# Kernel optimization log

Measured on AMD Instinct MI355X. Metric: run time of the kernel, lower is better.

## Reference

```python
import jax, jax.numpy as jnp
import numpy as np

B, T, F, H = 128, 256, 64, 512

def glorot(key, shape):
    fan_in, fan_out = shape[0], shape[1]
    lim = jnp.sqrt(6.0 / (fan_in + fan_out))
    return jax.random.uniform(key, shape, jnp.float32, -lim, lim)

def setup_inputs() -> dict:
    key = jax.random.key(0)
    ks = jax.random.split(key, 8)
    x = jax.random.normal(ks[0], (B, T, F), jnp.float32)
    W1 = glorot(ks[1], (F, H)); b1 = jnp.zeros((H,), jnp.float32)
    Wx1 = glorot(ks[2], (H, 4 * H)); Wh1 = glorot(ks[3], (H, 4 * H))
    blstm1 = jnp.concatenate([jnp.zeros((H,)), jnp.ones((H,)), jnp.zeros((2 * H,))]).astype(jnp.float32)  # keras unit_forget_bias
    Wx2 = glorot(ks[4], (H, 4 * H)); Wh2 = glorot(ks[5], (H, 4 * H))
    blstm2 = jnp.concatenate([jnp.zeros((H,)), jnp.ones((H,)), jnp.zeros((2 * H,))]).astype(jnp.float32)
    gamma = jnp.ones((H,), jnp.float32); beta = jnp.zeros((H,), jnp.float32)
    W2 = glorot(ks[6], (H, H // 2)); b2 = jnp.zeros((H // 2,), jnp.float32)
    W3 = glorot(ks[7], (H // 2, 1)); b3 = jnp.zeros((1,), jnp.float32)
    return dict(x=x, W1=W1, b1=b1, Wx1=Wx1, Wh1=Wh1, blstm1=blstm1,
                Wx2=Wx2, Wh2=Wh2, blstm2=blstm2, gamma=gamma, beta=beta,
                W2=W2, b2=b2, W3=W3, b3=b3)

def lstm(x, Wx, Wh, b):
    # x: [B, T, Din] -> sequence of hidden states [B, T, H] and last h [B, H]
    h_dim = Wh.shape[0]
    xg = jnp.einsum('btd,dg->btg', x, Wx) + b  # precompute input contributions [B,T,4H]
    def step(carry, xt):
        h, c = carry
        g = xt + h @ Wh
        i, f, cb, o = jnp.split(g, 4, axis=-1)
        i = jax.nn.sigmoid(i); f = jax.nn.sigmoid(f); o = jax.nn.sigmoid(o)
        c = f * c + i * jnp.tanh(cb)
        h = o * jnp.tanh(c)
        return (h, c), h
    init = (jnp.zeros((x.shape[0], h_dim), x.dtype), jnp.zeros((x.shape[0], h_dim), x.dtype))
    (h_last, _), hs = jax.lax.scan(step, init, jnp.swapaxes(xg, 0, 1))
    return jnp.swapaxes(hs, 0, 1), h_last

def reference(x, W1, b1, Wx1, Wh1, blstm1, Wx2, Wh2, blstm2, gamma, beta, W2, b2, W3, b3):
    h = x @ W1 + b1                                  # dense1 [B,T,H]
    # spectral_norm lambda: L2-normalize last axis, scale by sqrt(H)
    norm = jnp.linalg.norm(h, axis=-1, keepdims=True)
    h = h / jnp.maximum(norm, 1e-12) * jnp.sqrt(jnp.float32(h.shape[-1]))
    seq, _ = lstm(h, Wx1, Wh1, blstm1)               # lstm1 return_sequences
    _, h2 = lstm(seq, Wx2, Wh2, blstm2)              # lstm2 last output [B,H]
    mu = jnp.mean(h2, axis=-1, keepdims=True)
    var = jnp.mean((h2 - mu) ** 2, axis=-1, keepdims=True)
    h2 = (h2 - mu) * jax.lax.rsqrt(var + 1e-3) * gamma + beta  # keras LayerNorm eps=1e-3
    h3 = jax.nn.relu(h2 @ W2 + b2)
    return h3 @ W3 + b3                               # [B,1]
```

## Files before the change

kernel.cpp:

```cpp
#include <hip/hip_runtime.h>
#include <hip/hip_bf16.h>
#include <math.h>

#define B_ 128
#define T_ 256
#define F_ 64
#define H_ 512
#define G4_ 2048

#define XB0_OFF 0
#define XB1_OFF 32768
#define HB_OFF  65536
#define GLD_OFF 98304
#define SMEM_TOTAL 115712

typedef __attribute__((ext_vector_type(8))) short bf16x8;
typedef __attribute__((ext_vector_type(4))) float f32x4;

__device__ __forceinline__ void coh_store_u32(unsigned* p, unsigned v) {
  __hip_atomic_store(p, v, __ATOMIC_RELAXED, __HIP_MEMORY_SCOPE_AGENT);
}
__device__ __forceinline__ unsigned coh_load_u32(const unsigned* p) {
  return __hip_atomic_load(p, __ATOMIC_RELAXED, __HIP_MEMORY_SCOPE_AGENT);
}
__device__ __forceinline__ void rawbar() { __builtin_amdgcn_s_barrier(); }

__device__ __forceinline__ void async_ld16(const void* g, void* l) {
  __builtin_amdgcn_global_load_lds(
      (const __attribute__((address_space(1))) void*)g,
      (__attribute__((address_space(3))) void*)l, 16, 0, 0);
}
__device__ __forceinline__ void async_ld16c(const void* g, void* l) {
  __builtin_amdgcn_global_load_lds(
      (const __attribute__((address_space(1))) void*)g,
      (__attribute__((address_space(3))) void*)l, 16, 0, 17);
}

__device__ __forceinline__ float fsig(float x) {
  float e = __builtin_amdgcn_exp2f(-1.44269504089f * x);
  return __builtin_amdgcn_rcpf(1.f + e);
}
__device__ __forceinline__ float ftanh(float x) {
  float ax = __builtin_fabsf(x);
  float e = __builtin_amdgcn_exp2f(-2.88539008177f * ax);
  float r = (1.f - e) * __builtin_amdgcn_rcpf(1.f + e);
  return __builtin_copysignf(r, x);
}

__global__ __launch_bounds__(256) void transpose_cast_k(
    const float* __restrict__ s0, const float* __restrict__ s1,
    const float* __restrict__ s2, const float* __restrict__ s3,
    __hip_bfloat16* __restrict__ dst)
{
  __shared__ float lds[64][65];
  const float* src = (blockIdx.z == 0) ? s0 : (blockIdx.z == 1) ? s1 : (blockIdx.z == 2) ? s2 : s3;
  __hip_bfloat16* d = dst + (size_t)blockIdx.z * (G4_ * H_);
  int n0 = blockIdx.x * 64, k0 = blockIdx.y * 64;
  int tx = threadIdx.x & 63, ty = threadIdx.x >> 6;
#pragma unroll
  for (int r = 0; r < 16; r++) { int k = r * 4 + ty; lds[k][tx] = src[(size_t)(k0 + k) * G4_ + n0 + tx]; }
  __syncthreads();
#pragma unroll
  for (int r = 0; r < 16; r++) { int n = r * 4 + ty; d[(size_t)(n0 + n) * H_ + k0 + tx] = __float2bfloat16(lds[tx][n]); }
}

__global__ void prep_misc_k(const float* __restrict__ w1, __hip_bfloat16* __restrict__ w1b,
                            float* __restrict__ zbase, int nzero)
{
  int i = blockIdx.x * blockDim.x + threadIdx.x;
  int stride = gridDim.x * blockDim.x;
  for (int k = i; k < F_ * H_; k += stride) w1b[k] = __float2bfloat16(w1[k]);
  for (int k = i; k < nzero; k += stride) zbase[k] = 0.f;
}

__global__ __launch_bounds__(512) void dense1_k(
    const float* __restrict__ x, const __hip_bfloat16* __restrict__ w1b,
    const float* __restrict__ b1, __hip_bfloat16* __restrict__ h0)
{
  __shared__ float red[8];
  int j = threadIdx.x;
  int wave = j >> 6, lane = j & 63;
  float wcol[64];
#pragma unroll
  for (int k = 0; k < 64; k++) wcol[k] = __bfloat162float(w1b[k * H_ + j]);
  float bj = b1[j];
  for (int r = 0; r < 32; r++) {
    int row = blockIdx.x * 32 + r;
    const float* xr = x + (size_t)row * F_;
    float acc = bj;
#pragma unroll
    for (int k = 0; k < 64; k++) acc += xr[k] * wcol[k];
    float ss = acc * acc;
#pragma unroll
    for (int o = 32; o; o >>= 1) ss += __shfl_down(ss, o);
    if (lane == 0) red[wave] = ss;
    __syncthreads();
    float tot = red[0] + red[1] + red[2] + red[3] + red[4] + red[5] + red[6] + red[7];
    float sc = sqrtf(512.f) / fmaxf(sqrtf(tot), 1e-12f);
    h0[(size_t)row * H_ + j] = __float2bfloat16(acc * sc);
    __syncthreads();
  }
}

#define RUN_CHAIN(BASEPTR, W0, W1, A0, A1)                                    \
  {                                                                           \
    const char* _cb = (const char*)(BASEPTR);                                 \
    _Pragma("unroll")                                                         \
    for (int kc = 0; kc < 8; kc++) {                                          \
      bf16x8 _av = *(const bf16x8*)(_cb + ((mh * 16 + kh * 8 + kc) << 10) + (lane << 4)); \
      A0 = __builtin_amdgcn_mfma_f32_16x16x32_bf16(_av, W0[kc], A0, 0, 0, 0); \
      A1 = __builtin_amdgcn_mfma_f32_16x16x32_bf16(_av, W1[kc], A1, 0, 0, 0); \
    }                                                                         \
  }

__global__ __launch_bounds__(512, 2) void lstm_fused_k(
    const __hip_bfloat16* __restrict__ h0,
    __hip_bfloat16* __restrict__ seq,
    const __hip_bfloat16* __restrict__ wh1, const __hip_bfloat16* __restrict__ wx1,
    const float* __restrict__ bl1,
    const __hip_bfloat16* __restrict__ wh2, const __hip_bfloat16* __restrict__ wx2,
    const float* __restrict__ bl2,
    __hip_bfloat16* __restrict__ h1A, __hip_bfloat16* __restrict__ h1B,
    __hip_bfloat16* __restrict__ h2A, __hip_bfloat16* __restrict__ h2B,
    float* __restrict__ h2f,
    unsigned* flags)
{
  extern __shared__ char smem[];
  float* gld = (float*)(smem + GLD_OFF);
  const int tid = threadIdx.x;
  const int wave = tid >> 6;
  const int lane = tid & 63;
  const int lr = lane & 15;
  const int lk = lane >> 4;
  const int bid = blockIdx.x;
  const int grp = bid >> 7;
  const int lid = bid & 127;
  const int bb = lid & 3;
  const int bu = lid >> 2;
  const int m0 = bb * 32;
  const int u0 = bu * 16;

  const int kh = wave >> 2;
  const int mh = (wave >> 1) & 1;
  const int gp = wave & 1;

  const __hip_bfloat16* Wht = grp ? wh2 : wh1;
  const __hip_bfloat16* Wxt = grp ? wx2 : wx1;
  const __hip_bfloat16* xsrc = grp ? (const __hip_bfloat16*)seq : h0;
  const float* bias = grp ? bl2 : bl1;
  __hip_bfloat16* hgA = grp ? h2A : h1A;
  __hip_bfloat16* hgB = grp ? h2B : h1B;
  unsigned* dflags = flags + bb * 64;
  unsigned* ownf = dflags + (grp << 5);
  const int myflag = (grp << 5) | bu;

  bf16x8 wh_0[8], wh_1[8], wx_0[8], wx_1[8];
  {
    const size_t c0 = (size_t)((gp * 2 + 0) * 512 + u0 + lr) * H_ + kh * 256 + lk * 8;
    const size_t c1 = (size_t)((gp * 2 + 1) * 512 + u0 + lr) * H_ + kh * 256 + lk * 8;
#pragma unroll
    for (int kc = 0; kc < 8; kc++) {
      wh_0[kc] = *(const bf16x8*)(Wht + c0 + kc * 32);
      wh_1[kc] = *(const bf16x8*)(Wht + c1 + kc * 32);
      wx_0[kc] = *(const bf16x8*)(Wxt + c0 + kc * 32);
      wx_1[kc] = *(const bf16x8*)(Wxt + c1 + kc * 32);
    }
#pragma unroll
    for (int kc = 0; kc < 8; kc++) {
      asm volatile("" : "+v"(wh_0[kc]), "+v"(wh_1[kc]), "+v"(wx_0[kc]), "+v"(wx_1[kc]));
    }
  }

  const int m_e = tid >> 3, up_e = tid & 7;
  float br0[2], br1[2], br2[2], br3[2];
  float2 creg = {0.f, 0.f};
  if (tid < 256) {
#pragma unroll
    for (int c = 0; c < 2; c++) {
      br0[c] = bias[0 * 512 + u0 + 2 * up_e + c];
      br1[c] = bias[1 * 512 + u0 + 2 * up_e + c];
      br2[c] = bias[2 * 512 + u0 + 2 * up_e + c];
      br3[c] = bias[3 * 512 + u0 + 2 * up_e + c];
    }
  }

  char* xb0 = smem + XB0_OFF;
  char* xb1 = smem + XB1_OFF;

  auto issue_x = [&](int t, char* xb) {
#pragma unroll
    for (int j = 0; j < 4; j++) {
      const int c = wave * 4 + j;
      const __hip_bfloat16* g = xsrc +
          ((size_t)(m0 + (c >> 4) * 16 + lr) * T_ + t) * H_ + (c & 15) * 32 + lk * 8;
      if (grp) async_ld16c(g, xb + c * 1024);
      else     async_ld16(g, xb + c * 1024);
    }
  };
  auto issue_h = [&](const __hip_bfloat16* hsrc) {
#pragma unroll
    for (int j = 0; j < 4; j++) {
      const int c = wave * 4 + j;
      async_ld16c(hsrc + (size_t)(m0 + (c >> 4) * 16 + lr) * H_ + (c & 15) * 32 + lk * 8,
                  smem + HB_OFF + c * 1024);
    }
  };
  auto spin = [&](const unsigned* base, unsigned tgt) {
    if (lane < 32) {
      const unsigned* p = base + lane;
      while (coh_load_u32(p) < tgt) __builtin_amdgcn_s_sleep(2);
    }
  };
  auto publish = [&](unsigned v) {
    if (tid == 0) coh_store_u32(&dflags[myflag], v);
  };
  auto write_gld = [&](f32x4 s0, f32x4 s1) {
    float* d0 = gld + ((kh * 4 + gp * 2 + 0) * 32 + mh * 16 + lk * 4) * 17 + lr;
    float* d1 = gld + ((kh * 4 + gp * 2 + 1) * 32 + mh * 16 + lk * 4) * 17 + lr;
#pragma unroll
    for (int r = 0; r < 4; r++) { d0[r * 17] = s0[r]; d1[r * 17] = s1[r]; }
  };
  auto elem = [&](int u, __hip_bfloat16* hout) {
    if (tid < 256) {
      float gv0[2], gv1[2], gv2[2], gv3[2];
#pragma unroll
      for (int c = 0; c < 2; c++) {
        const int o = m_e * 17 + 2 * up_e + c;
        gv0[c] = gld[(0 * 32) * 17 + o] + gld[(4 * 32) * 17 + o] + br0[c];
        gv1[c] = gld[(1 * 32) * 17 + o] + gld[(5 * 32) * 17 + o] + br1[c];
        gv2[c] = gld[(2 * 32) * 17 + o] + gld[(6 * 32) * 17 + o] + br2[c];
        gv3[c] = gld[(3 * 32) * 17 + o] + gld[(7 * 32) * 17 + o] + br3[c];
      }
      float i0 = fsig(gv0[0]), i1 = fsig(gv0[1]);
      float f0 = fsig(gv1[0]), f1 = fsig(gv1[1]);
      float cb0 = ftanh(gv2[0]), cb1 = ftanh(gv2[1]);
      float o0 = fsig(gv3[0]), o1 = fsig(gv3[1]);
      float cn0 = f0 * creg.x + i0 * cb0;
      float cn1 = f1 * creg.y + i1 * cb1;
      creg.x = cn0; creg.y = cn1;
      float hv0 = o0 * ftanh(cn0), hv1 = o1 * ftanh(cn1);
      union { __hip_bfloat16 h[2]; unsigned u32; } pk;
      pk.h[0] = __float2bfloat16(hv0);
      pk.h[1] = __float2bfloat16(hv1);
      const int row = m0 + m_e, col = u0 + 2 * up_e;
      coh_store_u32((unsigned*)hout + ((size_t)row * H_ + col) / 2, pk.u32);
      if (grp == 0) {
        coh_store_u32((unsigned*)seq + (((size_t)row * T_ + u) * H_ + col) / 2, pk.u32);
      } else if (u == T_ - 1) {
        float2 hv = {hv0, hv1};
        *(float2*)(h2f + (size_t)row * H_ + col) = hv;
      }
    }
  };

  f32x4 axc0 = {0.f,0.f,0.f,0.f}, axc1 = {0.f,0.f,0.f,0.f};
  f32x4 axn0, axn1, ah0, ah1;

  if (grp) spin(dflags, 2u);
  issue_x(0, xb0);
  issue_x(1, xb1);
  asm volatile("s_waitcnt vmcnt(4)" ::: "memory");
  rawbar();
  __builtin_amdgcn_sched_barrier(0);
  RUN_CHAIN(xb0, wx_0, wx_1, axc0, axc1);
  write_gld(axc0, axc1);
  asm volatile("s_waitcnt lgkmcnt(0)" ::: "memory");
  rawbar();
  __builtin_amdgcn_sched_barrier(0);
  if (grp) spin(dflags, 3u);
  elem(0, hgA);
  issue_x(2, xb0);
  asm volatile("s_waitcnt vmcnt(4)" ::: "memory");
  rawbar();
  publish(1u);
  axc0 = (f32x4){0.f,0.f,0.f,0.f}; axc1 = (f32x4){0.f,0.f,0.f,0.f};
  RUN_CHAIN(xb1, wx_0, wx_1, axc0, axc1);

  for (int u = 1; u < T_; u++) {
    __hip_bfloat16* hsrc = ((u - 1) & 1) ? hgB : hgA;
    __hip_bfloat16* hout = (u & 1) ? hgB : hgA;
    const bool pf = (u <= T_ - 3);

    spin(ownf, (unsigned)u);
    issue_h(hsrc);
    if (grp && pf) spin(dflags, (unsigned)(u + 3));
    asm volatile("s_waitcnt vmcnt(4)" ::: "memory");
    rawbar();
    __builtin_amdgcn_sched_barrier(0);
    if (u < T_ - 1) {
      axn0 = (f32x4){0.f,0.f,0.f,0.f}; axn1 = (f32x4){0.f,0.f,0.f,0.f};
      char* xb = ((u + 1) & 1) ? xb1 : xb0;
      RUN_CHAIN(xb, wx_0, wx_1, axn0, axn1);
    }
    asm volatile("s_waitcnt vmcnt(0)" ::: "memory");
    rawbar();
    __builtin_amdgcn_sched_barrier(0);
    ah0 = (f32x4){0.f,0.f,0.f,0.f}; ah1 = (f32x4){0.f,0.f,0.f,0.f};
    RUN_CHAIN(smem + HB_OFF, wh_0, wh_1, ah0, ah1);
    write_gld(axc0 + ah0, axc1 + ah1);
    asm volatile("s_waitcnt lgkmcnt(0)" ::: "memory");
    rawbar();
    __builtin_amdgcn_sched_barrier(0);
    elem(u, hout);
    if (pf) {
      issue_x(u + 2, (u & 1) ? xb1 : xb0);
      asm volatile("s_waitcnt vmcnt(4)" ::: "memory");
    } else {
      asm volatile("s_waitcnt vmcnt(0)" ::: "memory");
    }
    rawbar();
    publish((unsigned)(u + 1));
    axc0 = axn0; axc1 = axn1;
  }
}

__global__ __launch_bounds__(256) void final_k(
    const float* __restrict__ h2, const float* __restrict__ gamma, const float* __restrict__ beta,
    const float* __restrict__ W2, const float* __restrict__ b2,
    const float* __restrict__ W3, const float* __restrict__ b3, float* __restrict__ out)
{
  __shared__ float y[512];
  __shared__ float redS[4], redQ[4], redP[4];
  int b = blockIdx.x, tid = threadIdx.x;
  int wave = tid >> 6, lane = tid & 63;
  float v0 = h2[b * H_ + tid], v1 = h2[b * H_ + 256 + tid];
  float s = v0 + v1, q = v0 * v0 + v1 * v1;
#pragma unroll
  for (int o = 32; o; o >>= 1) { s += __shfl_down(s, o); q += __shfl_down(q, o); }
  if (lane == 0) { redS[wave] = s; redQ[wave] = q; }
  __syncthreads();
  float tot = redS[0] + redS[1] + redS[2] + redS[3];
  float totq = redQ[0] + redQ[1] + redQ[2] + redQ[3];
  float mu = tot * (1.f / 512.f);
  float var = totq * (1.f / 512.f) - mu * mu;
  float rs = rsqrtf(var + 1e-3f);
  y[tid]       = (v0 - mu) * rs * gamma[tid] + beta[tid];
  y[tid + 256] = (v1 - mu) * rs * gamma[tid + 256] + beta[tid + 256];
  __syncthreads();
  float acc = b2[tid];
  for (int k = 0; k < 512; k++) acc += y[k] * W2[k * 256 + tid];
  float pv = fmaxf(acc, 0.f) * W3[tid];
#pragma unroll
  for (int o = 32; o; o >>= 1) pv += __shfl_down(pv, o);
  if (lane == 0) redP[wave] = pv;
  __syncthreads();
  if (tid == 0) out[b] = redP[0] + redP[1] + redP[2] + redP[3] + b3[0];
}

extern "C" void kernel_launch(void* const* d_in, const int* in_sizes, int n_in,
                              void* d_out, int out_size, void* d_ws, size_t ws_size,
                              hipStream_t stream)
{
  (void)in_sizes; (void)n_in; (void)out_size; (void)ws_size;
  const float* x    = (const float*)d_in[0];
  const float* W1   = (const float*)d_in[1];
  const float* b1   = (const float*)d_in[2];
  const float* Wx1  = (const float*)d_in[3];
  const float* Wh1  = (const float*)d_in[4];
  const float* bl1  = (const float*)d_in[5];
  const float* Wx2  = (const float*)d_in[6];
  const float* Wh2  = (const float*)d_in[7];
  const float* bl2  = (const float*)d_in[8];
  const float* gam  = (const float*)d_in[9];
  const float* bet  = (const float*)d_in[10];
  const float* W2   = (const float*)d_in[11];
  const float* b2   = (const float*)d_in[12];
  const float* W3   = (const float*)d_in[13];
  const float* b3   = (const float*)d_in[14];

  char* p = (char*)d_ws;
  const size_t MB = 1024 * 1024;
  __hip_bfloat16* wx1t = (__hip_bfloat16*)(p + 0 * MB);
  __hip_bfloat16* wh1t = (__hip_bfloat16*)(p + 2 * MB);
  __hip_bfloat16* wx2t = (__hip_bfloat16*)(p + 4 * MB);
  __hip_bfloat16* wh2t = (__hip_bfloat16*)(p + 6 * MB);
  __hip_bfloat16* w1b  = (__hip_bfloat16*)(p + 8 * MB);
  __hip_bfloat16* h0   = (__hip_bfloat16*)(p + 9 * MB);
  __hip_bfloat16* seq  = (__hip_bfloat16*)(p + 41 * MB);
  char* st = p + 73 * MB;
  __hip_bfloat16* h1A = (__hip_bfloat16*)st;
  __hip_bfloat16* h1B = h1A + B_ * H_;
  __hip_bfloat16* h2A = h1B + B_ * H_;
  __hip_bfloat16* h2B = h2A + B_ * H_;
  float* h2f = (float*)(st + 512 * 1024);
  unsigned* flags = (unsigned*)(st + 512 * 1024 + 256 * 1024);
  int nzero = (int)((512 * 1024 + 256 * 1024 + 4096) / 4);

  transpose_cast_k<<<dim3(32, 8, 4), 256, 0, stream>>>(Wx1, Wh1, Wx2, Wh2, wx1t);
  prep_misc_k<<<256, 256, 0, stream>>>(W1, w1b, (float*)st, nzero);
  dense1_k<<<1024, 512, 0, stream>>>(x, w1b, b1, h0);

  void* args[] = { (void*)&h0, (void*)&seq,
                   (void*)&wh1t, (void*)&wx1t, (void*)&bl1,
                   (void*)&wh2t, (void*)&wx2t, (void*)&bl2,
                   (void*)&h1A, (void*)&h1B, (void*)&h2A, (void*)&h2B,
                   (void*)&h2f, (void*)&flags };
  hipLaunchCooperativeKernel((void*)lstm_fused_k, dim3(256), dim3(512), args,
                             SMEM_TOTAL, stream);

  final_k<<<128, 256, 0, stream>>>(h2f, gam, bet, W2, b2, W3, b3, (float*)d_out);
}
```

Measured before the change: 1.331 ms.

## Streamline cross-block LSTM step handshake and drop duplicate layer-1 hidden store

Layer-1 blocks stop writing their hidden state to a separate ping-pong buffer; the recurrence input is now read straight from the seq output. The two per-step spin waits run in parallel on different lanes, and the spin sleep is shortened. Each step's flag is published before draining the outstanding x prefetch rather than after a full block barrier, and one barrier at the loop top is removed. This shortens the critical path of the inter-block step dependency, but publishing before the barrier risks exposing other waves' h stores before they are complete.

```diff
diff --git a/kernel.cpp b/kernel.cpp
--- a/kernel.cpp
+++ b/kernel.cpp
@@ -197,18 +197,36 @@
       else     async_ld16(g, xb + c * 1024);
     }
   };
-  auto issue_h = [&](const __hip_bfloat16* hsrc) {
+  auto issue_h = [&](int u) {
 #pragma unroll
     for (int j = 0; j < 4; j++) {
       const int c = wave * 4 + j;
-      async_ld16c(hsrc + (size_t)(m0 + (c >> 4) * 16 + lr) * H_ + (c & 15) * 32 + lk * 8,
-                  smem + HB_OFF + c * 1024);
-    }
-  };
-  auto spin = [&](const unsigned* base, unsigned tgt) {
+      const int row = m0 + (c >> 4) * 16 + lr;
+      const __hip_bfloat16* g;
+      if (grp) {
+        const __hip_bfloat16* hsrc = ((u - 1) & 1) ? hgB : hgA;
+        g = hsrc + (size_t)row * H_ + (c & 15) * 32 + lk * 8;
+      } else {
+        g = seq + ((size_t)row * T_ + (u - 1)) * H_ + (c & 15) * 32 + lk * 8;
+      }
+      async_ld16c(g, smem + HB_OFF + c * 1024);
+    }
+  };
+  auto spin32 = [&](const unsigned* base, unsigned tgt) {
     if (lane < 32) {
       const unsigned* p = base + lane;
-      while (coh_load_u32(p) < tgt) __builtin_amdgcn_s_sleep(2);
+      while (coh_load_u32(p) < tgt) __builtin_amdgcn_s_sleep(1);
+    }
+  };
+  auto spinA = [&](int u) {
+    if (lane < 32) {
+      const unsigned* p = ownf + lane;
+      const unsigned tgt = (unsigned)u;
+      while (coh_load_u32(p) < tgt) __builtin_amdgcn_s_sleep(1);
+    } else if (grp == 1 && u <= T_ - 3) {
+      const unsigned* p = dflags + (lane - 32);
+      const unsigned tgt = (unsigned)(u + 3);
+      while (coh_load_u32(p) < tgt) __builtin_amdgcn_s_sleep(1);
     }
   };
   auto publish = [&](unsigned v) {
@@ -243,12 +261,14 @@
       pk.h[0] = __float2bfloat16(hv0);
       pk.h[1] = __float2bfloat16(hv1);
       const int row = m0 + m_e, col = u0 + 2 * up_e;
-      coh_store_u32((unsigned*)hout + ((size_t)row * H_ + col) / 2, pk.u32);
       if (grp == 0) {
         coh_store_u32((unsigned*)seq + (((size_t)row * T_ + u) * H_ + col) / 2, pk.u32);
-      } else if (u == T_ - 1) {
-        float2 hv = {hv0, hv1};
-        *(float2*)(h2f + (size_t)row * H_ + col) = hv;
+      } else {
+        coh_store_u32((unsigned*)hout + ((size_t)row * H_ + col) / 2, pk.u32);
+        if (u == T_ - 1) {
+          float2 hv = {hv0, hv1};
+          *(float2*)(h2f + (size_t)row * H_ + col) = hv;
+        }
       }
     }
   };
@@ -256,10 +276,10 @@
   f32x4 axc0 = {0.f,0.f,0.f,0.f}, axc1 = {0.f,0.f,0.f,0.f};
   f32x4 axn0, axn1, ah0, ah1;
 
-  if (grp) spin(dflags, 2u);
+  if (grp) spin32(dflags, 3u);
   issue_x(0, xb0);
   issue_x(1, xb1);
-  asm volatile("s_waitcnt vmcnt(4)" ::: "memory");
+  asm volatile("s_waitcnt vmcnt(0)" ::: "memory");
   rawbar();
   __builtin_amdgcn_sched_barrier(0);
   RUN_CHAIN(xb0, wx_0, wx_1, axc0, axc1);
@@ -267,26 +287,22 @@
   asm volatile("s_waitcnt lgkmcnt(0)" ::: "memory");
   rawbar();
   __builtin_amdgcn_sched_barrier(0);
-  if (grp) spin(dflags, 3u);
   elem(0, hgA);
   issue_x(2, xb0);
   asm volatile("s_waitcnt vmcnt(4)" ::: "memory");
+  publish(1u);
+  asm volatile("s_waitcnt vmcnt(0)" ::: "memory");
   rawbar();
-  publish(1u);
+  __builtin_amdgcn_sched_barrier(0);
   axc0 = (f32x4){0.f,0.f,0.f,0.f}; axc1 = (f32x4){0.f,0.f,0.f,0.f};
   RUN_CHAIN(xb1, wx_0, wx_1, axc0, axc1);
 
   for (int u = 1; u < T_; u++) {
-    __hip_bfloat16* hsrc = ((u - 1) & 1) ? hgB : hgA;
     __hip_bfloat16* hout = (u & 1) ? hgB : hgA;
     const bool pf = (u <= T_ - 3);
 
-    spin(ownf, (unsigned)u);
-    issue_h(hsrc);
-    if (grp && pf) spin(dflags, (unsigned)(u + 3));
-    asm volatile("s_waitcnt vmcnt(4)" ::: "memory");
-    rawbar();
-    __builtin_amdgcn_sched_barrier(0);
+    spinA(u);
+    issue_h(u);
     if (u < T_ - 1) {
       axn0 = (f32x4){0.f,0.f,0.f,0.f}; axn1 = (f32x4){0.f,0.f,0.f,0.f};
       char* xb = ((u + 1) & 1) ? xb1 : xb0;
@@ -305,11 +321,13 @@
     if (pf) {
       issue_x(u + 2, (u & 1) ? xb1 : xb0);
       asm volatile("s_waitcnt vmcnt(4)" ::: "memory");
+      publish((unsigned)(u + 1));
+      asm volatile("s_waitcnt vmcnt(0)" ::: "memory");
     } else {
       asm volatile("s_waitcnt vmcnt(0)" ::: "memory");
+      publish((unsigned)(u + 1));
     }
     rawbar();
-    publish((unsigned)(u + 1));
     axc0 = axn0; axc1 = axn1;
   }
 }
```

Result: faster. 1.181 ms (-11.2%).
